# Performance work log

Measured on AMD Instinct MI355X. Metric: run time of the kernel, lower is better.

## Reference

```python
import jax, jax.numpy as jnp
import numpy as np

B, S, HID = 1, 2048, 4096
H, NOPE, ROPE, VD = 32, 128, 64, 128
QKD = NOPE + ROPE
Q_RANK, KV_RANK = 1536, 512
IDX_H, IDX_D, TOPK = 16, 128, 1024
EPS, THETA = 1e-5, 10000.0


def rmsnorm(x, w):
    return x * jax.lax.rsqrt(jnp.mean(x * x, axis=-1, keepdims=True) + EPS) * w


def rope_interleaved(x, pos):
    # x: [..., s, d]; rope_interleave=True -> rotate adjacent pairs
    d = x.shape[-1]
    inv_freq = 1.0 / (THETA ** (jnp.arange(0, d, 2, dtype=jnp.float32) / d))
    ang = pos[:, None] * inv_freq[None, :]  # [s, d/2]
    cos, sin = jnp.cos(ang), jnp.sin(ang)
    x2 = x.reshape(*x.shape[:-1], d // 2, 2)
    x0, x1 = x2[..., 0], x2[..., 1]
    return jnp.stack([x0 * cos - x1 * sin, x1 * cos + x0 * sin], axis=-1).reshape(x.shape)


def setup_inputs() -> dict:
    key = jax.random.key(0)
    ks = jax.random.split(key, 12)
    s = 0.02
    return {
        'hidden_states': jax.random.normal(ks[0], (B, S, HID), jnp.float32),
        'q_a_w': jax.random.normal(ks[1], (HID, Q_RANK), jnp.float32) * s,
        'q_a_norm_w': jnp.ones((Q_RANK,), jnp.float32),
        'q_b_w': jax.random.normal(ks[2], (Q_RANK, H * QKD), jnp.float32) * s,
        'kv_a_w': jax.random.normal(ks[3], (HID, KV_RANK + ROPE), jnp.float32) * s,
        'kv_a_norm_w': jnp.ones((KV_RANK,), jnp.float32),
        'kv_b_w': jax.random.normal(ks[4], (KV_RANK, H * (NOPE + VD)), jnp.float32) * s,
        'o_w': jax.random.normal(ks[5], (H * VD, HID), jnp.float32) * s,
        'idx_wq_w': jax.random.normal(ks[6], (HID, IDX_H * IDX_D), jnp.float32) * s,
        'idx_wk_w': jax.random.normal(ks[7], (HID, IDX_D), jnp.float32) * s,
        'idx_weights_w': jax.random.normal(ks[8], (HID, IDX_H), jnp.float32) * s,
    }


def reference(hidden_states, q_a_w, q_a_norm_w, q_b_w, kv_a_w, kv_a_norm_w,
              kv_b_w, o_w, idx_wq_w, idx_wk_w, idx_weights_w):
    b, s, _ = hidden_states.shape
    pos = jnp.arange(s, dtype=jnp.float32)

    # ---- MLA latent projections ----
    q_lat = rmsnorm(hidden_states @ q_a_w, q_a_norm_w)                 # [b,s,Q_RANK]
    q = (q_lat @ q_b_w).reshape(b, s, H, QKD).transpose(0, 2, 1, 3)    # [b,h,s,qkd]
    q_nope, q_pe = q[..., :NOPE], q[..., NOPE:]

    ckv = hidden_states @ kv_a_w                                       # [b,s,KV_RANK+ROPE]
    kv_lat, k_pe = ckv[..., :KV_RANK], ckv[..., KV_RANK:]
    kv = (rmsnorm(kv_lat, kv_a_norm_w) @ kv_b_w).reshape(b, s, H, NOPE + VD).transpose(0, 2, 1, 3)
    k_nope, v = kv[..., :NOPE], kv[..., NOPE:]

    q_pe = rope_interleaved(q_pe, pos)
    k_pe = rope_interleaved(k_pe[:, None, :, :], pos)                  # [b,1,s,ROPE] shared MQA rope head

    scores = (jnp.einsum('bhqd,bhkd->bhqk', q_nope, k_nope)
              + jnp.einsum('bhqd,bhkd->bhqk', q_pe, k_pe)) * (QKD ** -0.5)

    # ---- DSA lightning indexer: per-query top-k key selection ----
    iq = (hidden_states @ idx_wq_w).reshape(b, s, IDX_H, IDX_D)
    ik = hidden_states @ idx_wk_w                                      # [b,s,IDX_D]
    iw = (hidden_states @ idx_weights_w) * (IDX_H ** -0.5)             # [b,s,IDX_H]
    idx_scores = jnp.einsum('bqn,bnqk->bqk', iw,
                            jax.nn.relu(jnp.einsum('bqnd,bkd->bnqk', iq, ik))) * (IDX_D ** -0.5)
    causal = pos[:, None] >= pos[None, :]                              # [s,s]
    idx_scores = jnp.where(causal, idx_scores, -jnp.inf)
    _, topk_idx = jax.lax.top_k(idx_scores, TOPK)                      # [b,s,TOPK]
    bi = jnp.arange(b)[:, None, None]
    qi = jnp.arange(s)[None, :, None]
    topk_mask = jnp.zeros((b, s, s), bool).at[bi, qi, topk_idx].set(True)
    mask = topk_mask & causal                                          # [b,s,s]

    scores = jnp.where(mask[:, None], scores, -jnp.inf)
    attn = jax.nn.softmax(scores, axis=-1)
    out = jnp.einsum('bhqk,bhkd->bqhd', attn, v).reshape(b, s, H * VD)
    return out @ o_w
```

## Files before the change

kernel.cpp:

```cpp
#include <hip/hip_runtime.h>
#include <math.h>

#define S_LEN 2048
#define HIDDEN 4096
#define NHEAD 32
#define D_NOPE 128
#define D_ROPE 64
#define D_V 128
#define D_QK 192
#define QRANK 1536
#define KVRANK 512
#define IDXH 16
#define IDXD 128
#define KSEL 1024
#define NIDX 2304

typedef __attribute__((ext_vector_type(8))) short bf16x8;
typedef __attribute__((ext_vector_type(4))) float f32x4;
typedef __attribute__((ext_vector_type(4))) unsigned short u16x4;

__device__ __forceinline__ unsigned short f2b(float f) {
    union { float f; unsigned int u; } x; x.f = f;
    unsigned int r = x.u + 0x7FFFu + ((x.u >> 16) & 1u);
    return (unsigned short)(r >> 16);
}
__device__ __forceinline__ float b2f(unsigned short u) {
    union { unsigned int u; float f; } x; x.u = ((unsigned int)u) << 16; return x.f;
}

__device__ __forceinline__ void gload16(const void* g, const void* l) {
    __builtin_amdgcn_global_load_lds(
        (const __attribute__((address_space(1))) unsigned int*)(unsigned long long)g,
        (__attribute__((address_space(3))) unsigned int*)(unsigned int)(unsigned long long)l,
        16, 0, 0);
}

template <int OUT_BF16>
__global__ __launch_bounds__(256) void gemm_bf16(const unsigned short* __restrict__ A,
                                                 const unsigned short* __restrict__ Bt,
                                                 void* __restrict__ Cv,
                                                 int K, int ldc, float alpha) {
    __shared__ __align__(16) unsigned char lds[32768];
    const int tid = threadIdx.x;
    const int w = tid >> 6, lane = tid & 63;
    const int lr = lane & 15, g = lane >> 4;
    const int gx = gridDim.x;
    const int nwg = gx * gridDim.y;
    const int flat = blockIdx.y * gx + blockIdx.x;
    const int swz = (flat & 7) * (nwg >> 3) + (flat >> 3);
    const int bm = (swz / gx) * 128, bn = (swz % gx) * 128;
    const int wm = (w >> 1) * 64, wn = (w & 1) * 64;

    f32x4 acc[4][4];
#pragma unroll
    for (int i = 0; i < 4; ++i)
#pragma unroll
        for (int j = 0; j < 4; ++j) acc[i][j] = (f32x4){0.f, 0.f, 0.f, 0.f};

    int a_off[2], b_off[2];
#pragma unroll
    for (int issue = 0; issue < 2; ++issue) {
        const int off = issue * 4096 + w * 1024 + lane * 16;
        const int row = off >> 6, slot = (off >> 4) & 3;
        a_off[issue] = (bm + row) * K + ((slot ^ (row & 3)) << 3);
        b_off[issue] = (bn + row) * K + ((slot ^ (row & 3)) << 3);
    }

    const int KT = K >> 5;
    auto stage = [&](int t, int buf) {
        const int k0 = t << 5;
        unsigned char* l = lds + buf * 16384;
        gload16(A + a_off[0] + k0, l + w * 1024);
        gload16(A + a_off[1] + k0, l + 4096 + w * 1024);
        gload16(Bt + b_off[0] + k0, l + 8192 + w * 1024);
        gload16(Bt + b_off[1] + k0, l + 8192 + 4096 + w * 1024);
    };

    stage(0, 0);
    for (int t = 0; t < KT; ++t) {
        if (t + 1 < KT) {
            stage(t + 1, (t + 1) & 1);
            asm volatile("s_waitcnt vmcnt(4)" ::: "memory");
        } else {
            asm volatile("s_waitcnt vmcnt(0)" ::: "memory");
        }
        __syncthreads();
        const unsigned char* l = lds + (t & 1) * 16384;

        bf16x8 af[4], bfr[4];
#pragma unroll
        for (int i = 0; i < 4; ++i) {
            const int rowA = wm + i * 16 + lr;
            af[i] = *(const bf16x8*)(l + rowA * 64 + ((g ^ (rowA & 3)) << 4));
            const int rowB = wn + i * 16 + lr;
            bfr[i] = *(const bf16x8*)(l + 8192 + rowB * 64 + ((g ^ (rowB & 3)) << 4));
        }
#pragma unroll
        for (int i = 0; i < 4; ++i)
#pragma unroll
            for (int j = 0; j < 4; ++j)
                acc[i][j] = __builtin_amdgcn_mfma_f32_16x16x32_bf16(af[i], bfr[j], acc[i][j], 0, 0, 0);
        __syncthreads();
    }

#pragma unroll
    for (int i = 0; i < 4; ++i) {
        const int m = bm + wm + i * 16 + g * 4;
#pragma unroll
        for (int j = 0; j < 4; ++j) {
            const int n = bn + wn + j * 16 + lr;
            if (OUT_BF16) {
                unsigned short* Cb = (unsigned short*)Cv;
#pragma unroll
                for (int r = 0; r < 4; ++r)
                    Cb[(size_t)(m + r) * ldc + n] = f2b(acc[i][j][r] * alpha);
            } else {
                float* Cf = (float*)Cv;
#pragma unroll
                for (int r = 0; r < 4; ++r)
                    Cf[(size_t)(m + r) * ldc + n] = acc[i][j][r] * alpha;
            }
        }
    }
}

__global__ __launch_bounds__(256) void gemm_kvb(const unsigned short* __restrict__ A,
                                                const unsigned short* __restrict__ Bt,
                                                unsigned short* __restrict__ kb16,
                                                unsigned short* __restrict__ vT) {
    __shared__ __align__(16) unsigned char lds[34816];
    const int tid = threadIdx.x;
    const int w = tid >> 6, lane = tid & 63;
    const int lr = lane & 15, g = lane >> 4;
    const int gx = gridDim.x;
    const int nwg = gx * gridDim.y;
    const int flat = blockIdx.y * gx + blockIdx.x;
    const int swz = (flat & 7) * (nwg >> 3) + (flat >> 3);
    const int bm = (swz / gx) * 128, bn = (swz % gx) * 128;
    const int wm = (w >> 1) * 64, wn = (w & 1) * 64;
    const int K = KVRANK;

    f32x4 acc[4][4];
#pragma unroll
    for (int i = 0; i < 4; ++i)
#pragma unroll
        for (int j = 0; j < 4; ++j) acc[i][j] = (f32x4){0.f, 0.f, 0.f, 0.f};

    int a_off[2], b_off[2];
#pragma unroll
    for (int issue = 0; issue < 2; ++issue) {
        const int off = issue * 4096 + w * 1024 + lane * 16;
        const int row = off >> 6, slot = (off >> 4) & 3;
        a_off[issue] = (bm + row) * K + ((slot ^ (row & 3)) << 3);
        b_off[issue] = (bn + row) * K + ((slot ^ (row & 3)) << 3);
    }

    const int KT = K >> 5;
    auto stage = [&](int t, int buf) {
        const int k0 = t << 5;
        unsigned char* l = lds + buf * 16384;
        gload16(A + a_off[0] + k0, l + w * 1024);
        gload16(A + a_off[1] + k0, l + 4096 + w * 1024);
        gload16(Bt + b_off[0] + k0, l + 8192 + w * 1024);
        gload16(Bt + b_off[1] + k0, l + 8192 + 4096 + w * 1024);
    };

    stage(0, 0);
    for (int t = 0; t < KT; ++t) {
        if (t + 1 < KT) {
            stage(t + 1, (t + 1) & 1);
            asm volatile("s_waitcnt vmcnt(4)" ::: "memory");
        } else {
            asm volatile("s_waitcnt vmcnt(0)" ::: "memory");
        }
        __syncthreads();
        const unsigned char* l = lds + (t & 1) * 16384;

        bf16x8 af[4], bfr[4];
#pragma unroll
        for (int i = 0; i < 4; ++i) {
            const int rowA = wm + i * 16 + lr;
            af[i] = *(const bf16x8*)(l + rowA * 64 + ((g ^ (rowA & 3)) << 4));
            const int rowB = wn + i * 16 + lr;
            bfr[i] = *(const bf16x8*)(l + 8192 + rowB * 64 + ((g ^ (rowB & 3)) << 4));
        }
#pragma unroll
        for (int i = 0; i < 4; ++i)
#pragma unroll
            for (int j = 0; j < 4; ++j)
                acc[i][j] = __builtin_amdgcn_mfma_f32_16x16x32_bf16(af[i], bfr[j], acc[i][j], 0, 0, 0);
        __syncthreads();
    }

    const int h = bn >> 8;
    if ((bn & 128) == 0) {
#pragma unroll
        for (int i = 0; i < 4; ++i) {
            const int m = bm + wm + i * 16 + g * 4;
#pragma unroll
            for (int j = 0; j < 4; ++j) {
                const int dl = wn + j * 16 + lr;
#pragma unroll
                for (int r = 0; r < 4; ++r)
                    kb16[((size_t)h * S_LEN + m + r) * D_QK + dl] = f2b(acc[i][j][r]);
            }
        }
    } else {
        unsigned short(*T)[136] = (unsigned short(*)[136])lds;
#pragma unroll
        for (int i = 0; i < 4; ++i) {
            const int ml = wm + i * 16 + g * 4;
#pragma unroll
            for (int j = 0; j < 4; ++j) {
                const int dl = wn + j * 16 + lr;
#pragma unroll
                for (int r = 0; r < 4; ++r) T[dl][ml + r] = f2b(acc[i][j][r]);
            }
        }
        __syncthreads();
        const int row = tid >> 1, half = tid & 1;
        unsigned short* dst = vT + (size_t)(h * 128 + row) * S_LEN + bm + half * 64;
        const unsigned short* src = &T[row][half * 64];
#pragma unroll
        for (int u = 0; u < 8; ++u)
            *(uint4*)(dst + u * 8) = *(const uint4*)(src + u * 8);
    }
}

__global__ __launch_bounds__(256) void gemm_split(const unsigned short* __restrict__ Ah,
                                                  const unsigned short* __restrict__ Al,
                                                  const unsigned short* __restrict__ Bh,
                                                  const unsigned short* __restrict__ Bl,
                                                  float* __restrict__ C0,
                                                  float* __restrict__ C1) {
    const int K = HIDDEN, ldc = NIDX;
    const int bid = blockIdx.x;
    const int wf = (bid & 7) * 38 + (bid >> 3);
    const int kz = (wf >= 152) ? 1 : 0;
    const int wgid = wf - kz * 152;
    int x, y;
    if (wgid < 144) { y = 8 + wgid / 18; x = wgid % 18; }
    else            { x = 16; y = wgid - 144; }
    const int bm = y * 128, bn = x * 128;
    float* __restrict__ C = kz ? C1 : C0;

    __shared__ __align__(16) unsigned char lds[65536];
    const int tid = threadIdx.x;
    const int w = tid >> 6, lane = tid & 63;
    const int lr = lane & 15, g = lane >> 4;
    const int wm = (w >> 1) * 64, wn = (w & 1) * 64;

    f32x4 acc[4][4];
#pragma unroll
    for (int i = 0; i < 4; ++i)
#pragma unroll
        for (int j = 0; j < 4; ++j) acc[i][j] = (f32x4){0.f, 0.f, 0.f, 0.f};

    int a_off[2], b_off[2];
#pragma unroll
    for (int issue = 0; issue < 2; ++issue) {
        const int off = issue * 4096 + w * 1024 + lane * 16;
        const int row = off >> 6, slot = (off >> 4) & 3;
        a_off[issue] = (bm + row) * K + ((slot ^ (row & 3)) << 3) + kz * 2048;
        b_off[issue] = (bn + row) * K + ((slot ^ (row & 3)) << 3) + kz * 2048;
    }

    const int KT = 2048 >> 5;
    auto stage = [&](int t, int buf) {
        const int k0 = t << 5;
        unsigned char* l = lds + buf * 32768;
        gload16(Ah + a_off[0] + k0, l + w * 1024);
        gload16(Ah + a_off[1] + k0, l + 4096 + w * 1024);
        gload16(Al + a_off[0] + k0, l + 8192 + w * 1024);
        gload16(Al + a_off[1] + k0, l + 8192 + 4096 + w * 1024);
        gload16(Bh + b_off[0] + k0, l + 16384 + w * 1024);
        gload16(Bh + b_off[1] + k0, l + 16384 + 4096 + w * 1024);
        gload16(Bl + b_off[0] + k0, l + 24576 + w * 1024);
        gload16(Bl + b_off[1] + k0, l + 24576 + 4096 + w * 1024);
    };

    stage(0, 0);
    for (int t = 0; t < KT; ++t) {
        if (t + 1 < KT) {
            stage(t + 1, (t + 1) & 1);
            asm volatile("s_waitcnt vmcnt(8)" ::: "memory");
        } else {
            asm volatile("s_waitcnt vmcnt(0)" ::: "memory");
        }
        __syncthreads();
        const unsigned char* l = lds + (t & 1) * 32768;

        bf16x8 afh[4], afl[4], bfh[4], bfl[4];
#pragma unroll
        for (int i = 0; i < 4; ++i) {
            const int rowA = wm + i * 16 + lr;
            const int offA = rowA * 64 + ((g ^ (rowA & 3)) << 4);
            afh[i] = *(const bf16x8*)(l + offA);
            afl[i] = *(const bf16x8*)(l + 8192 + offA);
            const int rowB = wn + i * 16 + lr;
            const int offB = rowB * 64 + ((g ^ (rowB & 3)) << 4);
            bfh[i] = *(const bf16x8*)(l + 16384 + offB);
            bfl[i] = *(const bf16x8*)(l + 24576 + offB);
        }
#pragma unroll
        for (int i = 0; i < 4; ++i)
#pragma unroll
            for (int j = 0; j < 4; ++j) {
                acc[i][j] = __builtin_amdgcn_mfma_f32_16x16x32_bf16(afh[i], bfh[j], acc[i][j], 0, 0, 0);
                acc[i][j] = __builtin_amdgcn_mfma_f32_16x16x32_bf16(afh[i], bfl[j], acc[i][j], 0, 0, 0);
                acc[i][j] = __builtin_amdgcn_mfma_f32_16x16x32_bf16(afl[i], bfh[j], acc[i][j], 0, 0, 0);
            }
        __syncthreads();
    }

#pragma unroll
    for (int i = 0; i < 4; ++i) {
        const int m = bm + wm + i * 16 + g * 4;
#pragma unroll
        for (int j = 0; j < 4; ++j) {
            const int n = bn + wn + j * 16 + lr;
#pragma unroll
            for (int r = 0; r < 4; ++r)
                C[(size_t)(m + r) * ldc + n] = acc[i][j][r];
        }
    }
}

__global__ __launch_bounds__(256) void conv_split_h(const float* __restrict__ src,
                                                    unsigned short* __restrict__ dhi,
                                                    unsigned short* __restrict__ dlo) {
    const int i = blockIdx.x * 256 + threadIdx.x;
    const float4 v = ((const float4*)src)[i];
    u16x4 hi, lo;
    const float xs[4] = {v.x, v.y, v.z, v.w};
#pragma unroll
    for (int j = 0; j < 4; ++j) {
        const unsigned short h = f2b(xs[j]);
        hi[j] = h;
        lo[j] = f2b(xs[j] - b2f(h));
    }
    *(u16x4*)(dhi + (size_t)i * 4) = hi;
    *(u16x4*)(dlo + (size_t)i * 4) = lo;
}

__global__ __launch_bounds__(256) void conv_split_iq(const float* __restrict__ C0,
                                                     const float* __restrict__ C1,
                                                     unsigned short* __restrict__ iqh,
                                                     unsigned short* __restrict__ iql,
                                                     unsigned short* __restrict__ ikh,
                                                     unsigned short* __restrict__ ikl,
                                                     float* __restrict__ iwbuf) {
    const int i = blockIdx.x * 256 + threadIdx.x;
    const int row = i / 548, c4 = (i - row * 548) * 4;
    const float4 v0 = *(const float4*)(C0 + (size_t)row * NIDX + c4);
    const float4 v1 = *(const float4*)(C1 + (size_t)row * NIDX + c4);
    const float xs[4] = {v0.x + v1.x, v0.y + v1.y, v0.z + v1.z, v0.w + v1.w};
    if (c4 >= 2176) {
        *(float4*)(iwbuf + (size_t)row * 16 + (c4 - 2176)) =
            (float4){xs[0], xs[1], xs[2], xs[3]};
        return;
    }
    u16x4 hi, lo;
#pragma unroll
    for (int j = 0; j < 4; ++j) {
        const unsigned short h = f2b(xs[j]);
        hi[j] = h;
        lo[j] = f2b(xs[j] - b2f(h));
    }
    if (c4 < 2048) {
        *(u16x4*)(iqh + (size_t)row * 2048 + c4) = hi;
        *(u16x4*)(iql + (size_t)row * 2048 + c4) = lo;
    } else {
        *(u16x4*)(ikh + (size_t)row * 128 + c4 - 2048) = hi;
        *(u16x4*)(ikl + (size_t)row * 128 + c4 - 2048) = lo;
    }
}

__global__ __launch_bounds__(256) void wtrans(const float* __restrict__ W,
                                              unsigned short* __restrict__ Bt,
                                              int K, int Nsrc) {
    const int n0 = blockIdx.x * 64, k0 = blockIdx.y * 64;
    __shared__ unsigned short lv[64][72];
    const int tid = threadIdx.x;
#pragma unroll
    for (int it = 0; it < 16; ++it) {
        const int idx = tid + it * 256;
        const int kr = idx >> 6, n = idx & 63;
        const float v = (n0 + n < Nsrc) ? W[(size_t)(k0 + kr) * Nsrc + n0 + n] : 0.f;
        lv[n][kr] = f2b(v);
    }
    __syncthreads();
#pragma unroll
    for (int it = 0; it < 16; ++it) {
        const int idx = tid + it * 256;
        const int n = idx >> 6, kk = idx & 63;
        Bt[(size_t)(n0 + n) * K + k0 + kk] = lv[n][kk];
    }
}

__global__ __launch_bounds__(256) void wtrans_split(const float* __restrict__ W,
                                                    unsigned short* __restrict__ Bth,
                                                    unsigned short* __restrict__ Btl,
                                                    int K, int Nsrc) {
    const int n0 = blockIdx.x * 64, k0 = blockIdx.y * 64;
    __shared__ float lv[64][65];
    const int tid = threadIdx.x;
#pragma unroll
    for (int it = 0; it < 16; ++it) {
        const int idx = tid + it * 256;
        const int kr = idx >> 6, n = idx & 63;
        lv[n][kr] = (n0 + n < Nsrc) ? W[(size_t)(k0 + kr) * Nsrc + n0 + n] : 0.f;
    }
    __syncthreads();
#pragma unroll
    for (int it = 0; it < 16; ++it) {
        const int idx = tid + it * 256;
        const int n = idx >> 6, kk = idx & 63;
        const float x = lv[n][kk];
        const unsigned short h = f2b(x);
        Bth[(size_t)(n0 + n) * K + k0 + kk] = h;
        Btl[(size_t)(n0 + n) * K + k0 + kk] = f2b(x - b2f(h));
    }
}

__global__ __launch_bounds__(256) void rmsnormb(const float* __restrict__ in,
                                                const float* __restrict__ w,
                                                unsigned short* __restrict__ out,
                                                int W, int in_stride) {
    const int row = blockIdx.x;
    const int tid = threadIdx.x;
    const float* x = in + (size_t)row * in_stride;
    float ss = 0.f;
    for (int i = tid; i < W; i += 256) {
        float v = x[i];
        ss += v * v;
    }
    __shared__ float red[256];
    red[tid] = ss;
    __syncthreads();
    for (int s = 128; s > 0; s >>= 1) {
        if (tid < s) red[tid] += red[tid + s];
        __syncthreads();
    }
    const float scale = rsqrtf(red[0] / (float)W + 1e-5f);
    for (int i = tid; i < W; i += 256) out[(size_t)row * W + i] = f2b(x[i] * scale * w[i]);
}

__global__ __launch_bounds__(256) void rope_q16(unsigned short* __restrict__ q) {
    const int idx = blockIdx.x * 256 + threadIdx.x;
    if (idx >= S_LEN * NHEAD * (D_ROPE / 2)) return;
    const int i = idx & 31;
    const int h = (idx >> 5) & 31;
    const int s = idx >> 10;
    const float inv = __expf(-(float)i * (logf(10000.f) / 32.f));
    const float ang = (float)s * inv;
    const float cs = cosf(ang), sn = sinf(ang);
    unsigned short* p = q + (size_t)s * (NHEAD * D_QK) + h * D_QK + D_NOPE + 2 * i;
    const float x0 = b2f(p[0]), x1 = b2f(p[1]);
    p[0] = f2b(x0 * cs - x1 * sn);
    p[1] = f2b(x1 * cs + x0 * sn);
}

__global__ __launch_bounds__(256) void rope_k16b(const float* __restrict__ C1,
                                                 unsigned short* __restrict__ kb16) {
    const int idx = blockIdx.x * 256 + threadIdx.x;
    const int i = idx & 31;
    const int s = (idx >> 5) & 2047;
    const int h = idx >> 16;
    const float inv = __expf(-(float)i * (logf(10000.f) / 32.f));
    const float ang = (float)s * inv;
    const float cs = cosf(ang), sn = sinf(ang);
    const float* p = C1 + (size_t)s * 2176 + 2048 + 2 * i;
    const float x0 = p[0], x1 = p[1];
    unsigned short* o = kb16 + ((size_t)h * S_LEN + s) * D_QK + D_NOPE + 2 * i;
    o[0] = f2b(x0 * cs - x1 * sn);
    o[1] = f2b(x1 * cs + x0 * sn);
}

#define ISC_IKH 0
#define ISC_IKL 16384
#define ISC_IQH 32768
#define ISC_IQL 49152
#define ISC_IW 65536

__global__ __launch_bounds__(256) void idx_score_mfma(const unsigned short* __restrict__ iqh,
                                                      const unsigned short* __restrict__ iql,
                                                      const unsigned short* __restrict__ ikh,
                                                      const unsigned short* __restrict__ ikl,
                                                      const float* __restrict__ iwbuf,
                                                      float* __restrict__ iscore) {
    const int kt = blockIdx.x, qt = blockIdx.y + 16;
    if (kt > qt) return;
    const int q0 = qt * 64, k0 = kt * 64;
    __shared__ __align__(16) unsigned char smem[69632];
    const int tid = threadIdx.x;
    const int w = tid >> 6, lane = tid & 63;
    const int g = lane >> 4, lr = lane & 15;

#pragma unroll
    for (int it = 0; it < 4; ++it) {
        const int j = tid + it * 256;
        const int row = j >> 4, slot = j & 15;
        const int dst = row * 256 + ((slot ^ (row & 7)) << 4);
        *(uint4*)(smem + ISC_IKH + dst) = *(const uint4*)(ikh + (size_t)(k0 + row) * 128 + slot * 8);
        *(uint4*)(smem + ISC_IKL + dst) = *(const uint4*)(ikl + (size_t)(k0 + row) * 128 + slot * 8);
    }
    {
        const int r = tid >> 2, c4 = (tid & 3) * 4;
        const float4 v = *(const float4*)(iwbuf + (size_t)(q0 + r) * 16 + c4);
        float4 sv = {v.x * 0.25f, v.y * 0.25f, v.z * 0.25f, v.w * 0.25f};
        *(float4*)(smem + ISC_IW + r * 64 + c4 * 4) = sv;
    }

    f32x4 tot[4];
#pragma unroll
    for (int j = 0; j < 4; ++j) tot[j] = (f32x4){0.f, 0.f, 0.f, 0.f};

    for (int n = 0; n < IDXH; ++n) {
        __syncthreads();
#pragma unroll
        for (int it = 0; it < 4; ++it) {
            const int j = tid + it * 256;
            const int row = j >> 4, slot = j & 15;
            const int dst = row * 256 + ((slot ^ (row & 7)) << 4);
            *(uint4*)(smem + ISC_IQH + dst) =
                *(const uint4*)(iqh + (size_t)(q0 + row) * 2048 + n * 128 + slot * 8);
            *(uint4*)(smem + ISC_IQL + dst) =
                *(const uint4*)(iql + (size_t)(q0 + row) * 2048 + n * 128 + slot * 8);
        }
        __syncthreads();

        bf16x8 aH[4], aL[4];
        const int ar = w * 16 + lr;
#pragma unroll
        for (int kk = 0; kk < 4; ++kk) {
            const int off = ar * 256 + (((kk * 4 + g) ^ (ar & 7)) << 4);
            aH[kk] = *(const bf16x8*)(smem + ISC_IQH + off);
            aL[kk] = *(const bf16x8*)(smem + ISC_IQL + off);
        }
        float wv[4];
#pragma unroll
        for (int r = 0; r < 4; ++r)
            wv[r] = *(const float*)(smem + ISC_IW + (w * 16 + g * 4 + r) * 64 + n * 4);

#pragma unroll
        for (int jj = 0; jj < 4; ++jj) {
            f32x4 s = (f32x4){0.f, 0.f, 0.f, 0.f};
#pragma unroll
            for (int kk = 0; kk < 4; ++kk) {
                const int br = jj * 16 + lr;
                const int off = br * 256 + (((kk * 4 + g) ^ (br & 7)) << 4);
                const bf16x8 bH = *(const bf16x8*)(smem + ISC_IKH + off);
                const bf16x8 bL = *(const bf16x8*)(smem + ISC_IKL + off);
                s = __builtin_amdgcn_mfma_f32_16x16x32_bf16(aH[kk], bH, s, 0, 0, 0);
                s = __builtin_amdgcn_mfma_f32_16x16x32_bf16(aH[kk], bL, s, 0, 0, 0);
                s = __builtin_amdgcn_mfma_f32_16x16x32_bf16(aL[kk], bH, s, 0, 0, 0);
            }
#pragma unroll
            for (int r = 0; r < 4; ++r) tot[jj][r] += wv[r] * fmaxf(s[r], 0.f);
        }
    }

    const float sc = 0.08838834764831845f;
#pragma unroll
    for (int jj = 0; jj < 4; ++jj)
#pragma unroll
        for (int r = 0; r < 4; ++r)
            iscore[(size_t)(q0 + w * 16 + g * 4 + r) * S_LEN + k0 + jj * 16 + lr] =
                tot[jj][r] * sc;
}

__global__ __launch_bounds__(256) void topk_kernel(const float* __restrict__ iscore,
                                                   unsigned char* __restrict__ maskb) {
    const int q = blockIdx.x;
    const int tid = threadIdx.x;
    const int nk = q + 1;
    unsigned char* mrow = maskb + (size_t)q * 256;
    if (nk <= KSEL) {
        unsigned char b = 0;
#pragma unroll
        for (int bi = 0; bi < 8; ++bi)
            if (tid * 8 + bi <= q) b |= (unsigned char)(1 << bi);
        mrow[tid] = b;
        return;
    }
    __shared__ unsigned int uv[S_LEN];
    __shared__ unsigned int hist[256];
    __shared__ unsigned int sh_pfx, sh_rem;
    const float* srow = iscore + (size_t)q * S_LEN;
    for (int k = tid; k < nk; k += 256) {
        unsigned int b = __float_as_uint(srow[k]);
        uv[k] = (b & 0x80000000u) ? ~b : (b | 0x80000000u);
    }
    if (tid == 0) { sh_pfx = 0u; sh_rem = KSEL; }
    __syncthreads();

    const int lane = tid & 63;
#pragma unroll
    for (int shift = 24; shift >= 0; shift -= 8) {
        const unsigned int pfx = sh_pfx;
        const unsigned int rem = sh_rem;
        const unsigned int pmask = (shift == 24) ? 0u : (0xFFFFFFFFu << (shift + 8));
        hist[tid] = 0u;
        __syncthreads();
        for (int k = tid; k < nk; k += 256) {
            const unsigned int u = uv[k];
            if ((u & pmask) == pfx)
                atomicAdd(&hist[(u >> shift) & 255u], 1u);
        }
        __syncthreads();
        const unsigned int h0 = hist[lane * 4], h1 = hist[lane * 4 + 1];
        const unsigned int h2 = hist[lane * 4 + 2], h3 = hist[lane * 4 + 3];
        unsigned int sufp = h0 + h1 + h2 + h3;
#pragma unroll
        for (int off = 1; off < 64; off <<= 1) {
            const unsigned int o = __shfl_down(sufp, off);
            if (lane + off < 64) sufp += o;
        }
        unsigned int run = __shfl_down(sufp, 1);
        if (lane == 63) run = 0u;
        const unsigned int s3 = run + h3;
        const unsigned int s2 = s3 + h2;
        const unsigned int s1 = s2 + h1;
        const unsigned int s0 = s1 + h0;
        int bsel = -1;
        unsigned int gt = 0u;
        if (s3 >= rem && run < rem)      { bsel = 3; gt = run; }
        else if (s2 >= rem && s3 < rem)  { bsel = 2; gt = s3; }
        else if (s1 >= rem && s2 < rem)  { bsel = 1; gt = s2; }
        else if (s0 >= rem && s1 < rem)  { bsel = 0; gt = s1; }
        if (bsel >= 0) {
            sh_pfx = pfx | ((unsigned int)(lane * 4 + bsel) << shift);
            sh_rem = rem - gt;
        }
        __syncthreads();
    }
    const unsigned int T = sh_pfx;
    const int r = (int)sh_rem;
    unsigned char b = 0;
#pragma unroll
    for (int bi = 0; bi < 8; ++bi) {
        const int k = tid * 8 + bi;
        if (k < nk) {
            const unsigned int u = uv[k];
            if (u > T) {
                b |= (unsigned char)(1 << bi);
            } else if (u == T) {
                int rank = 0;
                for (int j = 0; j < k; ++j) rank += (uv[j] == T) ? 1 : 0;
                if (rank < r) b |= (unsigned char)(1 << bi);
            }
        }
    }
    mrow[tid] = b;
}

#define KVB 64
#define AQB 128
#define AT_K0 0
#define AT_V0 49152
#define AT_TOT 81920

__global__ __launch_bounds__(512) void attn_mfma_kernel(
    const unsigned short* __restrict__ qbuf16,
    const unsigned short* __restrict__ kb16,
    const unsigned short* __restrict__ vT,
    const unsigned char* __restrict__ maskb,
    unsigned short* __restrict__ ab16) {
    __shared__ __align__(16) unsigned char smem[AT_TOT];
    const int bid = blockIdx.x;
    const int xcd = bid & 7, jj = bid >> 3;
    const int h = (xcd << 2) | (jj & 3);
    const int qt = 15 - (jj >> 2);
    const int q0 = qt * AQB;
    const int tid = threadIdx.x;
    const int w = tid >> 6, lane = tid & 63;
    const int g = lane >> 4, lr = lane & 15;
    const int wub = (tid & ~63) * 16;

    const unsigned char* kbase = (const unsigned char*)(kb16 + (size_t)h * S_LEN * D_QK);
    const unsigned char* vbase = (const unsigned char*)(vT + (size_t)h * 128 * S_LEN);
    const unsigned char* mbase = maskb + (size_t)q0 * 256;

    bf16x8 qf[6];
    {
        const unsigned short* qrow =
            qbuf16 + (size_t)(q0 + w * 16 + lr) * (NHEAD * D_QK) + h * D_QK;
#pragma unroll
        for (int c = 0; c < 6; ++c) qf[c] = *(const bf16x8*)(qrow + c * 32 + g * 8);
    }

    auto stageK = [&](int k0, int kb) {
#pragma unroll
        for (int it = 0; it < 3; ++it) {
            const int j = tid + it * 512;
            const int row = j / 24, cs = j - row * 24;
            const int scs = (cs & ~7) | ((cs & 7) ^ (row & 7));
            gload16(kbase + (size_t)(k0 + row) * 384 + scs * 16, smem + kb + it * 8192 + wub);
        }
    };
    auto stageV = [&](int k0, int vb) {
#pragma unroll
        for (int it = 0; it < 2; ++it) {
            const int j = tid + it * 512;
            const int d = j >> 3, sl = j & 7;
            gload16(vbase + ((size_t)d * S_LEN + k0) * 2 + ((sl ^ (d & 7)) * 16),
                    smem + vb + it * 8192 + wub);
        }
    };

    f32x4 O[8];
#pragma unroll
    for (int db = 0; db < 8; ++db) O[db] = (f32x4){0.f, 0.f, 0.f, 0.f};
    float mS[4] = {-INFINITY, -INFINITY, -INFINITY, -INFINITY};
    float lS[4] = {0.f, 0.f, 0.f, 0.f};

    const int nt = 2 * qt + 2;
    stageK(0, AT_K0);
    stageV(0, AT_V0);
    asm volatile("s_waitcnt vmcnt(0)" ::: "memory");
    __syncthreads();

    for (int t = 0; t < nt; ++t) {
        const int cK = AT_K0 + (t & 1) * 24576;
        const int cV = AT_V0 + (t & 1) * 16384;
        uint2 mreg[4];
#pragma unroll
        for (int r = 0; r < 4; ++r)
            mreg[r] = *(const uint2*)(mbase + (size_t)(w * 16 + g * 4 + r) * 256 + t * 8);
        if (t + 1 < nt) {
            stageK((t + 1) * KVB, AT_K0 + (((t + 1) & 1)) * 24576);
            stageV((t + 1) * KVB, AT_V0 + (((t + 1) & 1)) * 16384);
        }

        f32x4 a[4];
#pragma unroll
        for (int j = 0; j < 4; ++j) a[j] = (f32x4){0.f, 0.f, 0.f, 0.f};
        __builtin_amdgcn_s_setprio(1);
#pragma unroll
        for (int c = 0; c < 6; ++c) {
            const int s = c * 4 + g;
#pragma unroll
            for (int j = 0; j < 4; ++j) {
                const int row = j * 16 + lr;
                const int scs = (s & ~7) | ((s & 7) ^ (lr & 7));
                const bf16x8 b = *(const bf16x8*)(smem + cK + row * 384 + scs * 16);
                a[j] = __builtin_amdgcn_mfma_f32_16x16x32_bf16(qf[c], b, a[j], 0, 0, 0);
            }
        }
        __builtin_amdgcn_s_setprio(0);

        __builtin_amdgcn_sched_barrier(0);
        asm volatile("s_barrier" ::: "memory");
        __builtin_amdgcn_sched_barrier(0);
        unsigned short* Pw = (unsigned short*)(smem + cK + w * 2304);

        float corr[4];
#pragma unroll
        for (int r = 0; r < 4; ++r) {
            const unsigned int mlo = mreg[r].x, mhi = mreg[r].y;
            float sv[4];
            sv[0] = ((mlo >> lr) & 1u) ? a[0][r] : -INFINITY;
            sv[1] = ((mlo >> (lr + 16)) & 1u) ? a[1][r] : -INFINITY;
            sv[2] = ((mhi >> lr) & 1u) ? a[2][r] : -INFINITY;
            sv[3] = ((mhi >> (lr + 16)) & 1u) ? a[3][r] : -INFINITY;
            float tm = fmaxf(fmaxf(sv[0], sv[1]), fmaxf(sv[2], sv[3]));
            tm = fmaxf(tm, __shfl_xor(tm, 1));
            tm = fmaxf(tm, __shfl_xor(tm, 2));
            tm = fmaxf(tm, __shfl_xor(tm, 4));
            tm = fmaxf(tm, __shfl_xor(tm, 8));
            const float mn = fmaxf(mS[r], tm);
            const float co = (mS[r] > -INFINITY) ? __expf(mS[r] - mn) : 0.f;
            float p[4];
#pragma unroll
            for (int j = 0; j < 4; ++j) p[j] = (sv[j] > -INFINITY) ? __expf(sv[j] - mn) : 0.f;
            float rs = (p[0] + p[1]) + (p[2] + p[3]);
            rs += __shfl_xor(rs, 1);
            rs += __shfl_xor(rs, 2);
            rs += __shfl_xor(rs, 4);
            rs += __shfl_xor(rs, 8);
            lS[r] = lS[r] * co + rs;
            mS[r] = mn;
            corr[r] = co;
#pragma unroll
            for (int j = 0; j < 4; ++j) Pw[(g * 4 + r) * 72 + j * 16 + lr] = f2b(p[j]);
        }
#pragma unroll
        for (int r = 0; r < 4; ++r) {
            if (corr[r] != 1.0f) {
#pragma unroll
                for (int db = 0; db < 8; ++db) O[db][r] *= corr[r];
            }
        }

        asm volatile("s_waitcnt lgkmcnt(0)" ::: "memory");
        __builtin_amdgcn_sched_barrier(0);

        __builtin_amdgcn_s_setprio(1);
#pragma unroll
        for (int c2 = 0; c2 < 2; ++c2) {
            const bf16x8 pA = *(const bf16x8*)((const unsigned char*)Pw + lr * 144 + c2 * 64 + g * 16);
#pragma unroll
            for (int db = 0; db < 8; ++db) {
                const int d = db * 16 + lr;
                const int s2 = c2 * 4 + g;
                const bf16x8 bV = *(const bf16x8*)(smem + cV + d * 128 + ((s2 ^ (d & 7)) << 4));
                O[db] = __builtin_amdgcn_mfma_f32_16x16x32_bf16(pA, bV, O[db], 0, 0, 0);
            }
        }
        __builtin_amdgcn_s_setprio(0);

        asm volatile("s_waitcnt vmcnt(0)" ::: "memory");
        __syncthreads();
    }

#pragma unroll
    for (int r = 0; r < 4; ++r) {
        const float inv = (lS[r] > 0.f) ? 1.f / lS[r] : 0.f;
        const int qg = q0 + w * 16 + g * 4 + r;
        unsigned short* orow = ab16 + (size_t)qg * (NHEAD * D_V) + h * D_V;
#pragma unroll
        for (int db = 0; db < 8; ++db) orow[db * 16 + lr] = f2b(O[db][r] * inv);
    }
}

extern "C" void kernel_launch(void* const* d_in, const int* in_sizes, int n_in,
                              void* d_out, int out_size, void* d_ws, size_t ws_size,
                              hipStream_t stream) {
    const float* hidden        = (const float*)d_in[0];
    const float* q_a_w         = (const float*)d_in[1];
    const float* q_a_norm_w    = (const float*)d_in[2];
    const float* q_b_w         = (const float*)d_in[3];
    const float* kv_a_w        = (const float*)d_in[4];
    const float* kv_a_norm_w   = (const float*)d_in[5];
    const float* kv_b_w        = (const float*)d_in[6];
    const float* o_w           = (const float*)d_in[7];
    const float* idx_wq_w      = (const float*)d_in[8];
    const float* idx_wk_w      = (const float*)d_in[9];
    const float* idx_weights_w = (const float*)d_in[10];
    float* out = (float*)d_out;

    char* ws = (char*)d_ws;
    unsigned short* BtAll = (unsigned short*)(ws + 0);
    unsigned short* owT   = (unsigned short*)(ws + 0);
    unsigned short* h16    = (unsigned short*)(ws + 33554432);
    unsigned short* h_lo   = (unsigned short*)(ws + 50331648);
    unsigned short* qbuf16 = (unsigned short*)(ws + 33554432);
    float* C1          = (float*)(ws + 67108864);
    unsigned short* vT = (unsigned short*)(ws + 67108864);
    unsigned short* BtIdxH = (unsigned short*)(ws + 84934656);
    unsigned short* BtIdxL = (unsigned short*)(ws + 103809024);
    unsigned short* kb16   = (unsigned short*)(ws + 84934656);
    float* Cidx         = (float*)(ws + 122683392);
    unsigned short* qbT = (unsigned short*)(ws + 122683392);
    unsigned short* iqh  = (unsigned short*)(ws + 141557760);
    unsigned short* iql  = (unsigned short*)(ws + 149946368);
    unsigned short* ikh  = (unsigned short*)(ws + 158334976);
    unsigned short* ikl  = (unsigned short*)(ws + 158859264);
    unsigned short* kvbT = (unsigned short*)(ws + 141557760);
    float* iscr          = (float*)(ws + 159383552);
    unsigned short* ab16 = (unsigned short*)(ws + 159383552);
    unsigned char* maskb  = (unsigned char*)(ws + 176160768);
    unsigned short* qa16  = (unsigned short*)(ws + 180355072);
    unsigned short* kvn16 = (unsigned short*)(ws + 186646528);
    float* iwbuf = (float*)(ws + 189005824);
    float* Cidx2 = (float*)(ws + 189136896);
    (void)ws_size; (void)in_sizes; (void)n_in; (void)out_size;

    const dim3 blk(256);
    const float QK_SCALE = 0.07216878364870323f;

    conv_split_h<<<8192, blk, 0, stream>>>(hidden, h16, h_lo);

    wtrans<<<dim3(24, 64), blk, 0, stream>>>(q_a_w, BtAll, HIDDEN, QRANK);
    wtrans<<<dim3(9, 64), blk, 0, stream>>>(kv_a_w, BtAll + (size_t)1536 * HIDDEN, HIDDEN, KVRANK + D_ROPE);
    wtrans<<<dim3(1, 64), blk, 0, stream>>>(q_a_w, BtAll + (size_t)2112 * HIDDEN, HIDDEN, 0);
    gemm_bf16<0><<<dim3(17, 16), blk, 0, stream>>>(h16, BtAll, C1, HIDDEN, 2176, 1.f);

    rmsnormb<<<S_LEN, blk, 0, stream>>>(C1, q_a_norm_w, qa16, QRANK, 2176);
    rmsnormb<<<S_LEN, blk, 0, stream>>>(C1 + 1536, kv_a_norm_w, kvn16, KVRANK, 2176);

    wtrans_split<<<dim3(32, 64), blk, 0, stream>>>(idx_wq_w, BtIdxH, BtIdxL, HIDDEN, IDXH * IDXD);
    wtrans_split<<<dim3(2, 64), blk, 0, stream>>>(idx_wk_w, BtIdxH + (size_t)2048 * HIDDEN,
                                                  BtIdxL + (size_t)2048 * HIDDEN, HIDDEN, IDXD);
    wtrans_split<<<dim3(2, 64), blk, 0, stream>>>(idx_weights_w, BtIdxH + (size_t)2176 * HIDDEN,
                                                  BtIdxL + (size_t)2176 * HIDDEN, HIDDEN, IDXH);
    gemm_split<<<dim3(304), blk, 0, stream>>>(h16, h_lo, BtIdxH, BtIdxL, Cidx, Cidx2);
    conv_split_iq<<<4384, blk, 0, stream>>>(Cidx, Cidx2, iqh, iql, ikh, ikl, iwbuf);
    idx_score_mfma<<<dim3(32, 16), blk, 0, stream>>>(iqh, iql, ikh, ikl, iwbuf, iscr);
    topk_kernel<<<S_LEN, blk, 0, stream>>>(iscr, maskb);

    rope_k16b<<<(NHEAD * S_LEN * 32) / 256, blk, 0, stream>>>(C1, kb16);

    wtrans<<<dim3(96, 24), blk, 0, stream>>>(q_b_w, qbT, QRANK, NHEAD * D_QK);
    wtrans<<<dim3(128, 8), blk, 0, stream>>>(kv_b_w, kvbT, KVRANK, NHEAD * 256);
    gemm_bf16<1><<<dim3(48, 16), blk, 0, stream>>>(qa16, qbT, qbuf16, QRANK, NHEAD * D_QK, QK_SCALE);
    gemm_kvb<<<dim3(64, 16), blk, 0, stream>>>(kvn16, kvbT, kb16, vT);
    rope_q16<<<(S_LEN * NHEAD * 32 + 255) / 256, blk, 0, stream>>>(qbuf16);

    attn_mfma_kernel<<<dim3(512), dim3(512), 0, stream>>>(qbuf16, kb16, vT, maskb, ab16);

    wtrans<<<dim3(64, 64), blk, 0, stream>>>(o_w, owT, NHEAD * D_V, HIDDEN);
    gemm_bf16<0><<<dim3(32, 16), blk, 0, stream>>>(ab16, owT, out, NHEAD * D_V, HIDDEN, 1.f);
}
```

Baseline: 768.8 us.

## Preload attention mask tile into LDS and give P its own buffer

The attention kernel now copies the whole 128-row mask tile into shared memory once at kernel start instead of issuing per-tile global loads for mask words. P is written to a dedicated LDS region rather than reusing the current K buffer, which removes the mid-iteration s_barrier. The conditional rescale of O is replaced by an unconditional multiply. LDS use grows from 80 KB to 130 KB per block, which may limit occupancy. The initial mask gload has no explicit wait before first use except the existing vmcnt(0).

```diff
diff --git a/kernel.cpp b/kernel.cpp
--- a/kernel.cpp
+++ b/kernel.cpp
@@ -659,7 +659,9 @@
 #define AQB 128
 #define AT_K0 0
 #define AT_V0 49152
-#define AT_TOT 81920
+#define AT_P 81920
+#define AT_M 100352
+#define AT_TOT 133120
 
 __global__ __launch_bounds__(512) void attn_mfma_kernel(
     const unsigned short* __restrict__ qbuf16,
@@ -690,6 +692,12 @@
         for (int c = 0; c < 6; ++c) qf[c] = *(const bf16x8*)(qrow + c * 32 + g * 8);
     }
 
+#pragma unroll
+    for (int it = 0; it < 4; ++it) {
+        const int j = tid + it * 512;
+        gload16(mbase + (size_t)j * 16, smem + AT_M + it * 8192 + wub);
+    }
+
     auto stageK = [&](int k0, int kb) {
 #pragma unroll
         for (int it = 0; it < 3; ++it) {
@@ -714,6 +722,7 @@
     for (int db = 0; db < 8; ++db) O[db] = (f32x4){0.f, 0.f, 0.f, 0.f};
     float mS[4] = {-INFINITY, -INFINITY, -INFINITY, -INFINITY};
     float lS[4] = {0.f, 0.f, 0.f, 0.f};
+    unsigned short* Pw = (unsigned short*)(smem + AT_P + w * 2304);
 
     const int nt = 2 * qt + 2;
     stageK(0, AT_K0);
@@ -724,13 +733,9 @@
     for (int t = 0; t < nt; ++t) {
         const int cK = AT_K0 + (t & 1) * 24576;
         const int cV = AT_V0 + (t & 1) * 16384;
-        uint2 mreg[4];
-#pragma unroll
-        for (int r = 0; r < 4; ++r)
-            mreg[r] = *(const uint2*)(mbase + (size_t)(w * 16 + g * 4 + r) * 256 + t * 8);
         if (t + 1 < nt) {
-            stageK((t + 1) * KVB, AT_K0 + (((t + 1) & 1)) * 24576);
-            stageV((t + 1) * KVB, AT_V0 + (((t + 1) & 1)) * 16384);
+            stageK((t + 1) * KVB, AT_K0 + ((t + 1) & 1) * 24576);
+            stageV((t + 1) * KVB, AT_V0 + ((t + 1) & 1) * 16384);
         }
 
         f32x4 a[4];
@@ -750,15 +755,13 @@
         }
         __builtin_amdgcn_s_setprio(0);
 
-        __builtin_amdgcn_sched_barrier(0);
-        asm volatile("s_barrier" ::: "memory");
-        __builtin_amdgcn_sched_barrier(0);
-        unsigned short* Pw = (unsigned short*)(smem + cK + w * 2304);
-
+        const int moff = (t * KVB) >> 3;
         float corr[4];
 #pragma unroll
         for (int r = 0; r < 4; ++r) {
-            const unsigned int mlo = mreg[r].x, mhi = mreg[r].y;
+            const int qrl = w * 16 + g * 4 + r;
+            const unsigned int mlo = *(const unsigned int*)(smem + AT_M + qrl * 256 + moff);
+            const unsigned int mhi = *(const unsigned int*)(smem + AT_M + qrl * 256 + moff + 4);
             float sv[4];
             sv[0] = ((mlo >> lr) & 1u) ? a[0][r] : -INFINITY;
             sv[1] = ((mlo >> (lr + 16)) & 1u) ? a[1][r] : -INFINITY;
@@ -786,11 +789,11 @@
             for (int j = 0; j < 4; ++j) Pw[(g * 4 + r) * 72 + j * 16 + lr] = f2b(p[j]);
         }
 #pragma unroll
-        for (int r = 0; r < 4; ++r) {
-            if (corr[r] != 1.0f) {
-#pragma unroll
-                for (int db = 0; db < 8; ++db) O[db][r] *= corr[r];
-            }
+        for (int db = 0; db < 8; ++db) {
+            O[db][0] *= corr[0];
+            O[db][1] *= corr[1];
+            O[db][2] *= corr[2];
+            O[db][3] *= corr[3];
         }
 
         asm volatile("s_waitcnt lgkmcnt(0)" ::: "memory");
```

After: 750.5 us (median of 2 runs). 2.4% less time.

## Single-buffer V and load it within the iteration to cut attention LDS

Applied to the files above, without the earlier changes.

The attention kernel now double-buffers only K. V for the current tile is issued at the start of each iteration and waited on with a partial vmcnt and a barrier just before the PV MFMAs. This cuts shared memory from 80KB to 64KB, which may let more blocks fit per CU, and overlaps the V load with the QK and softmax work. It also makes the O rescaling unconditional and branch-free. The cost is that the V load latency is exposed whenever it is not hidden by the QK/softmax phase, and each iteration gains an extra barrier.

```diff
diff --git a/kernel.cpp b/kernel.cpp
--- a/kernel.cpp
+++ b/kernel.cpp
@@ -657,9 +657,10 @@
 
 #define KVB 64
 #define AQB 128
-#define AT_K0 0
-#define AT_V0 49152
-#define AT_TOT 81920
+#define AT_KA 0
+#define AT_KB 24576
+#define AT_V 49152
+#define AT_TOT 65536
 
 __global__ __launch_bounds__(512) void attn_mfma_kernel(
     const unsigned short* __restrict__ qbuf16,
@@ -699,13 +700,13 @@
             gload16(kbase + (size_t)(k0 + row) * 384 + scs * 16, smem + kb + it * 8192 + wub);
         }
     };
-    auto stageV = [&](int k0, int vb) {
+    auto stageV = [&](int k0) {
 #pragma unroll
         for (int it = 0; it < 2; ++it) {
             const int j = tid + it * 512;
             const int d = j >> 3, sl = j & 7;
             gload16(vbase + ((size_t)d * S_LEN + k0) * 2 + ((sl ^ (d & 7)) * 16),
-                    smem + vb + it * 8192 + wub);
+                    smem + AT_V + it * 8192 + wub);
         }
     };
 
@@ -716,22 +717,20 @@
     float lS[4] = {0.f, 0.f, 0.f, 0.f};
 
     const int nt = 2 * qt + 2;
-    stageK(0, AT_K0);
-    stageV(0, AT_V0);
+    stageK(0, AT_KA);
     asm volatile("s_waitcnt vmcnt(0)" ::: "memory");
     __syncthreads();
 
     for (int t = 0; t < nt; ++t) {
-        const int cK = AT_K0 + (t & 1) * 24576;
-        const int cV = AT_V0 + (t & 1) * 16384;
+        const int cK = (t & 1) ? AT_KB : AT_KA;
+        const int nK = (t & 1) ? AT_KA : AT_KB;
         uint2 mreg[4];
 #pragma unroll
         for (int r = 0; r < 4; ++r)
             mreg[r] = *(const uint2*)(mbase + (size_t)(w * 16 + g * 4 + r) * 256 + t * 8);
-        if (t + 1 < nt) {
-            stageK((t + 1) * KVB, AT_K0 + (((t + 1) & 1)) * 24576);
-            stageV((t + 1) * KVB, AT_V0 + (((t + 1) & 1)) * 16384);
-        }
+        __builtin_amdgcn_sched_barrier(0);
+        stageV(t * KVB);
+        if (t + 1 < nt) stageK((t + 1) * KVB, nK);
 
         f32x4 a[4];
 #pragma unroll
@@ -786,14 +785,23 @@
             for (int j = 0; j < 4; ++j) Pw[(g * 4 + r) * 72 + j * 16 + lr] = f2b(p[j]);
         }
 #pragma unroll
-        for (int r = 0; r < 4; ++r) {
-            if (corr[r] != 1.0f) {
-#pragma unroll
-                for (int db = 0; db < 8; ++db) O[db][r] *= corr[r];
-            }
+        for (int db = 0; db < 8; ++db) {
+            O[db][0] *= corr[0];
+            O[db][1] *= corr[1];
+            O[db][2] *= corr[2];
+            O[db][3] *= corr[3];
         }
 
         asm volatile("s_waitcnt lgkmcnt(0)" ::: "memory");
+        __builtin_amdgcn_sched_barrier(0);
+
+        if (t + 1 < nt) {
+            asm volatile("s_waitcnt vmcnt(3)" ::: "memory");
+        } else {
+            asm volatile("s_waitcnt vmcnt(0)" ::: "memory");
+        }
+        __builtin_amdgcn_sched_barrier(0);
+        asm volatile("s_barrier" ::: "memory");
         __builtin_amdgcn_sched_barrier(0);
 
         __builtin_amdgcn_s_setprio(1);
@@ -804,7 +812,7 @@
             for (int db = 0; db < 8; ++db) {
                 const int d = db * 16 + lr;
                 const int s2 = c2 * 4 + g;
-                const bf16x8 bV = *(const bf16x8*)(smem + cV + d * 128 + ((s2 ^ (d & 7)) << 4));
+                const bf16x8 bV = *(const bf16x8*)(smem + AT_V + d * 128 + ((s2 ^ (d & 7)) << 4));
                 O[db] = __builtin_amdgcn_mfma_f32_16x16x32_bf16(pA, bV, O[db], 0, 0, 0);
             }
         }
```

New measurement: 761.8 us. About the same (-0.9%).
